# Optimization experiments

Hardware: AMD Instinct MI355X
Metric: run time of the kernel (lower is better)

Reference implementation:

```python
import jax, jax.numpy as jnp
import numpy as np

N = 100000      # nodes
E = 1600000     # edges (avg degree 16)
F_IN = 128
F_OUT = 128
EPS = 1e-5      # BatchNorm eps


def setup_inputs() -> dict:
    key = jax.random.key(0)
    ks = jax.random.split(key, 10)
    s_in = 1.0 / np.sqrt(F_IN)
    s_out = 1.0 / np.sqrt(F_OUT)
    return {
        "x": jax.random.normal(ks[0], (N, F_IN), dtype=jnp.float32),
        "edge_index": jax.random.randint(ks[1], (2, E), 0, N, dtype=jnp.int32),
        # layer 0: SAGEConv(F_IN, F_OUT, aggr='max'); lin_l has bias, lin_r does not
        "W0_l": jax.random.normal(ks[2], (F_IN, F_OUT), dtype=jnp.float32) * s_in,
        "b0_l": jnp.zeros((F_OUT,), dtype=jnp.float32),
        "W0_r": jax.random.normal(ks[3], (F_IN, F_OUT), dtype=jnp.float32) * s_in,
        "gamma0": jnp.ones((F_OUT,), dtype=jnp.float32),
        "beta0": jnp.zeros((F_OUT,), dtype=jnp.float32),
        # layer 1: SAGEConv(F_OUT, F_OUT, aggr='max')
        "W1_l": jax.random.normal(ks[4], (F_OUT, F_OUT), dtype=jnp.float32) * s_out,
        "b1_l": jnp.zeros((F_OUT,), dtype=jnp.float32),
        "W1_r": jax.random.normal(ks[5], (F_OUT, F_OUT), dtype=jnp.float32) * s_out,
        "gamma1": jnp.ones((F_OUT,), dtype=jnp.float32),
        "beta1": jnp.zeros((F_OUT,), dtype=jnp.float32),
    }


def _sage_conv_max(x, src, dst, W_l, b_l, W_r):
    # gather source features along edges, scatter-max into destination nodes
    msgs = x[src]                                             # [E, F]
    agg = jax.ops.segment_max(msgs, dst, num_segments=N)      # [N, F], -inf for isolated
    agg = jnp.where(jnp.isfinite(agg), agg, 0.0)              # PyG fills empty segments with 0
    return agg @ W_l + b_l + x @ W_r                          # lin_l(aggr) + lin_r(x)


def _batch_norm(h, gamma, beta):
    mu = jnp.mean(h, axis=0)
    var = jnp.var(h, axis=0)
    return (h - mu) * jax.lax.rsqrt(var + EPS) * gamma + beta


def reference(x, edge_index, W0_l, b0_l, W0_r, gamma0, beta0,
              W1_l, b1_l, W1_r, gamma1, beta1):
    src, dst = edge_index[0], edge_index[1]
    h = _sage_conv_max(x, src, dst, W0_l, b0_l, W0_r)
    h = jax.nn.relu(_batch_norm(h, gamma0, beta0))
    h = _sage_conv_max(h, src, dst, W1_l, b1_l, W1_r)
    h = jax.nn.relu(_batch_norm(h, gamma1, beta1))
    return h
```

## Files before the change

### kernel.cpp

```cpp
#include <hip/hip_runtime.h>
#include <stdint.h>

#define EPS_BN 1e-5f

typedef __attribute__((ext_vector_type(8))) short short8v;
typedef __attribute__((ext_vector_type(4))) float f32x4;

__device__ __forceinline__ unsigned rne_bf16(float f) {
    unsigned u = __float_as_uint(f);
    return (u + 0x7FFFu + ((u >> 16) & 1u)) >> 16;
}

extern "C" __global__ __launch_bounds__(256)
void f32_to_bf16_kernel(const float4* __restrict__ in, uint2* __restrict__ out, long n4) {
    long i = (long)blockIdx.x * 256 + threadIdx.x;
    long stride = (long)gridDim.x * 256;
    for (; i < n4; i += stride) {
        float4 v = in[i];
        uint2 o;
        o.x = rne_bf16(v.x) | (rne_bf16(v.y) << 16);
        o.y = rne_bf16(v.z) | (rne_bf16(v.w) << 16);
        out[i] = o;
    }
}

extern "C" __global__ __launch_bounds__(256)
void wt_prep2_kernel(const float* __restrict__ Wl0, const float* __restrict__ Wr0,
                     unsigned short* __restrict__ Wt0,
                     const float* __restrict__ Wl1, const float* __restrict__ Wr1,
                     unsigned short* __restrict__ Wt1) {
    int b = blockIdx.x;
    const float* Wl = (b < 128) ? Wl0 : Wl1;
    const float* Wr = (b < 128) ? Wr0 : Wr1;
    unsigned short* Wt = (b < 128) ? Wt0 : Wt1;
    int idx = (b & 127) * 256 + threadIdx.x;
    int col = idx >> 8, k = idx & 255;
    float v = (k < 128) ? Wl[(size_t)k * 128 + col] : Wr[(size_t)(k - 128) * 128 + col];
    Wt[(size_t)col * 256 + k] = (unsigned short)rne_bf16(v);
}

extern "C" __global__ __launch_bounds__(256)
void init_head_kernel(int* __restrict__ head, int n) {
    int i = blockIdx.x * 256 + threadIdx.x;
    if (i < n) head[i] = -1;
}

extern "C" __global__ __launch_bounds__(256)
void link_kernel(const int* __restrict__ ei, int* __restrict__ head4,
                 uint2* __restrict__ pair, int E) {
    int e = blockIdx.x * 256 + threadIdx.x;
    if (e < E) {
        int src = ei[e];
        int dst = ei[E + e];
        int old = atomicExch(&head4[dst * 4 + (e & 3)], e);
        uint2 p; p.x = (unsigned)src; p.y = (unsigned)old;
        pair[e] = p;
    }
}

#define FM8(v)                                              \
    a0 = fmaxf(a0, __uint_as_float((v).x << 16));           \
    a1 = fmaxf(a1, __uint_as_float((v).x));                 \
    a2 = fmaxf(a2, __uint_as_float((v).y << 16));           \
    a3 = fmaxf(a3, __uint_as_float((v).y));                 \
    a4 = fmaxf(a4, __uint_as_float((v).z << 16));           \
    a5 = fmaxf(a5, __uint_as_float((v).z));                 \
    a6 = fmaxf(a6, __uint_as_float((v).w << 16));           \
    a7 = fmaxf(a7, __uint_as_float((v).w));

extern "C" __global__ __launch_bounds__(256, 8)
void gather_max_ll16_kernel(const uint4* __restrict__ x16r, const int* __restrict__ head4,
                            const uint2* __restrict__ pair,
                            uint4* __restrict__ agg16, float* __restrict__ stats, int Nn) {
    if (blockIdx.x == 0 && threadIdx.x < 256) stats[threadIdx.x] = 0.0f;
    int t = blockIdx.x * 256 + threadIdx.x;
    int node = t >> 4;
    if (node >= Nn) return;
    int lane = t & 15;

    int4 hh = *(const int4*)(head4 + (size_t)node * 4);
    int e0 = hh.x, e1 = hh.y, e2 = hh.z, e3 = hh.w;

    uint4 out;
    if ((e0 & e1 & e2 & e3) < 0 && e0 < 0 && e1 < 0 && e2 < 0 && e3 < 0) {
        out.x = out.y = out.z = out.w = 0u;
    } else {
        float a0 = -INFINITY, a1 = -INFINITY, a2 = -INFINITY, a3 = -INFINITY;
        float a4 = -INFINITY, a5 = -INFINITY, a6 = -INFINITY, a7 = -INFINITY;
        while ((e0 & e1 & e2 & e3) >= 0 || e0 >= 0 || e1 >= 0 || e2 >= 0 || e3 >= 0) {
            bool b0 = e0 >= 0, b1 = e1 >= 0, b2 = e2 >= 0, b3 = e3 >= 0;
            uint2 p0, p1, p2, p3;
            uint4 v0, v1, v2, v3;
            if (b0) p0 = pair[e0];
            if (b1) p1 = pair[e1];
            if (b2) p2 = pair[e2];
            if (b3) p3 = pair[e3];
            if (b0) v0 = x16r[(size_t)p0.x * 16 + lane];
            if (b1) v1 = x16r[(size_t)p1.x * 16 + lane];
            if (b2) v2 = x16r[(size_t)p2.x * 16 + lane];
            if (b3) v3 = x16r[(size_t)p3.x * 16 + lane];
            if (b0) { e0 = (int)p0.y; FM8(v0); }
            if (b1) { e1 = (int)p1.y; FM8(v1); }
            if (b2) { e2 = (int)p2.y; FM8(v2); }
            if (b3) { e3 = (int)p3.y; FM8(v3); }
        }
        out.x = (__float_as_uint(a0) >> 16) | (__float_as_uint(a1) & 0xFFFF0000u);
        out.y = (__float_as_uint(a2) >> 16) | (__float_as_uint(a3) & 0xFFFF0000u);
        out.z = (__float_as_uint(a4) >> 16) | (__float_as_uint(a5) & 0xFFFF0000u);
        out.w = (__float_as_uint(a6) >> 16) | (__float_as_uint(a7) & 0xFFFF0000u);
    }
    agg16[(size_t)node * 16 + lane] = out;
}

extern "C" __global__ __launch_bounds__(256)
void gemm_bf16_kernel(const unsigned short* __restrict__ agg16,
                      const unsigned short* __restrict__ xin16,
                      const unsigned short* __restrict__ Wt,
                      const float* __restrict__ bias,
                      float* __restrict__ h, float* __restrict__ stats, int nrows) {
    __shared__ float redS[4][128];
    __shared__ float redQ[4][128];

    const int t = threadIdx.x;
    const int w = t >> 6, l = t & 63;
    const int wm = w >> 1, wn = w & 1;
    const int r16 = l & 15, g = l >> 4;
    const int blockRow = blockIdx.x * 128;
    const int colBase = wn * 64;

    f32x4 acc[4][4];
#pragma unroll
    for (int m = 0; m < 4; ++m)
#pragma unroll
        for (int n = 0; n < 4; ++n) acc[m][n] = (f32x4){0.f, 0.f, 0.f, 0.f};

    const short8v az = {0, 0, 0, 0, 0, 0, 0, 0};

#pragma unroll
    for (int kt = 0; kt < 8; ++kt) {
        const unsigned short* Asrc = (kt < 4) ? agg16 : xin16;
        const int kofs = (kt < 4) ? kt * 32 : kt * 32 - 128;

        short8v b[4];
#pragma unroll
        for (int n = 0; n < 4; ++n) {
            int col = colBase + n * 16 + r16;
            b[n] = *(const short8v*)(Wt + (size_t)col * 256 + kt * 32 + g * 8);
        }
        short8v a[4];
#pragma unroll
        for (int m = 0; m < 4; ++m) {
            int row = blockRow + wm * 64 + m * 16 + r16;
            a[m] = (row < nrows)
                 ? *(const short8v*)(Asrc + (size_t)row * 128 + kofs + g * 8)
                 : az;
        }
#pragma unroll
        for (int m = 0; m < 4; ++m)
#pragma unroll
            for (int n = 0; n < 4; ++n)
                acc[m][n] = __builtin_amdgcn_mfma_f32_16x16x32_bf16(a[m], b[n], acc[m][n], 0, 0, 0);
    }

    for (int i = t; i < 512; i += 256) {
        ((float*)redS)[i] = 0.f;
        ((float*)redQ)[i] = 0.f;
    }
    __syncthreads();

    float bcol[4];
#pragma unroll
    for (int n = 0; n < 4; ++n) bcol[n] = bias[colBase + n * 16 + r16];

    float s4[4] = {0.f, 0.f, 0.f, 0.f};
    float q4[4] = {0.f, 0.f, 0.f, 0.f};
#pragma unroll
    for (int m = 0; m < 4; ++m) {
#pragma unroll
        for (int reg = 0; reg < 4; ++reg) {
            int row = blockRow + wm * 64 + m * 16 + g * 4 + reg;
            if (row < nrows) {
#pragma unroll
                for (int n = 0; n < 4; ++n) {
                    float o = acc[m][n][reg] + bcol[n];
                    h[(size_t)row * 128 + colBase + n * 16 + r16] = o;
                    s4[n] += o;
                    q4[n] += o * o;
                }
            }
        }
    }
#pragma unroll
    for (int n = 0; n < 4; ++n) {
        s4[n] += __shfl_xor(s4[n], 16, 64);
        s4[n] += __shfl_xor(s4[n], 32, 64);
        q4[n] += __shfl_xor(q4[n], 16, 64);
        q4[n] += __shfl_xor(q4[n], 32, 64);
    }
    if (g == 0) {
#pragma unroll
        for (int n = 0; n < 4; ++n) {
            redS[w][colBase + n * 16 + r16] = s4[n];
            redQ[w][colBase + n * 16 + r16] = q4[n];
        }
    }
    __syncthreads();
    if (t < 128) {
        float s = redS[0][t] + redS[1][t] + redS[2][t] + redS[3][t];
        float q = redQ[0][t] + redQ[1][t] + redQ[2][t] + redQ[3][t];
        atomicAdd(&stats[t], s);
        atomicAdd(&stats[128 + t], q);
    }
}

__device__ __forceinline__ void bn_make_ss(const float* __restrict__ stats,
                                           const float* __restrict__ gamma,
                                           const float* __restrict__ beta,
                                           float inv_n, float* s_ss) {
    int t = threadIdx.x;
    if (t < 128) {
        float mu = stats[t] * inv_n;
        float var = stats[128 + t] * inv_n - mu * mu;
        float sc = gamma[t] * rsqrtf(var + EPS_BN);
        s_ss[t] = sc;
        s_ss[128 + t] = beta[t] - mu * sc;
    }
    __syncthreads();
}

extern "C" __global__ __launch_bounds__(256)
void bn_relu_tobf16_kernel(const float4* __restrict__ h, const float* __restrict__ stats,
                           const float* __restrict__ gamma, const float* __restrict__ beta,
                           float inv_n, uint2* __restrict__ y16, long n4) {
    __shared__ float s_ss[256];
    bn_make_ss(stats, gamma, beta, inv_n, s_ss);
    long i = (long)blockIdx.x * blockDim.x + threadIdx.x;
    long stride = (long)gridDim.x * blockDim.x;
    for (; i < n4; i += stride) {
        int c4 = (int)(i & 31) * 4;
        float4 v = h[i];
        float o0 = fmaxf(fmaf(v.x, s_ss[c4 + 0], s_ss[128 + c4 + 0]), 0.f);
        float o1 = fmaxf(fmaf(v.y, s_ss[c4 + 1], s_ss[128 + c4 + 1]), 0.f);
        float o2 = fmaxf(fmaf(v.z, s_ss[c4 + 2], s_ss[128 + c4 + 2]), 0.f);
        float o3 = fmaxf(fmaf(v.w, s_ss[c4 + 3], s_ss[128 + c4 + 3]), 0.f);
        uint2 o;
        o.x = rne_bf16(o0) | (rne_bf16(o1) << 16);
        o.y = rne_bf16(o2) | (rne_bf16(o3) << 16);
        y16[i] = o;
    }
}

extern "C" __global__ __launch_bounds__(256)
void bn_relu_f32_kernel(float4* __restrict__ h, const float* __restrict__ stats,
                        const float* __restrict__ gamma, const float* __restrict__ beta,
                        float inv_n, long n4) {
    __shared__ float s_ss[256];
    bn_make_ss(stats, gamma, beta, inv_n, s_ss);
    long i = (long)blockIdx.x * blockDim.x + threadIdx.x;
    long stride = (long)gridDim.x * blockDim.x;
    for (; i < n4; i += stride) {
        int c4 = (int)(i & 31) * 4;
        float4 v = h[i];
        v.x = fmaxf(fmaf(v.x, s_ss[c4 + 0], s_ss[128 + c4 + 0]), 0.f);
        v.y = fmaxf(fmaf(v.y, s_ss[c4 + 1], s_ss[128 + c4 + 1]), 0.f);
        v.z = fmaxf(fmaf(v.z, s_ss[c4 + 2], s_ss[128 + c4 + 2]), 0.f);
        v.w = fmaxf(fmaf(v.w, s_ss[c4 + 3], s_ss[128 + c4 + 3]), 0.f);
        h[i] = v;
    }
}

__device__ __forceinline__ unsigned map_f(float f) {
    unsigned u = __float_as_uint(f);
    return (u & 0x80000000u) ? ~u : (u | 0x80000000u);
}
__device__ __forceinline__ float unmap_f(unsigned m) {
    return (m & 0x80000000u) ? __uint_as_float(m & 0x7FFFFFFFu) : __uint_as_float(~m);
}

extern "C" __global__ __launch_bounds__(256)
void init_sentinel_kernel(uint4* __restrict__ agg, long n4) {
    uint4 z = {0u, 0u, 0u, 0u};
    long i = (long)blockIdx.x * blockDim.x + threadIdx.x;
    long stride = (long)gridDim.x * blockDim.x;
    for (; i < n4; i += stride) agg[i] = z;
}

extern "C" __global__ __launch_bounds__(256)
void scatter_max_kernel(const float4* __restrict__ xin, const int* __restrict__ ei,
                        unsigned* __restrict__ agg, int E) {
    int t = blockIdx.x * 256 + threadIdx.x;
    int e = t >> 5;
    if (e >= E) return;
    int f4 = t & 31;
    int src = ei[e];
    int dst = ei[E + e];
    float4 v = xin[(size_t)src * 32 + f4];
    unsigned* p = agg + (size_t)dst * 128 + (size_t)f4 * 4;
    atomicMax(p + 0, map_f(v.x));
    atomicMax(p + 1, map_f(v.y));
    atomicMax(p + 2, map_f(v.z));
    atomicMax(p + 3, map_f(v.w));
}

extern "C" __global__ __launch_bounds__(256)
void unmap_kernel(unsigned* __restrict__ agg, long n) {
    long i = (long)blockIdx.x * blockDim.x + threadIdx.x;
    long stride = (long)gridDim.x * blockDim.x;
    for (; i < n; i += stride) {
        unsigned u = agg[i];
        agg[i] = __float_as_uint(u ? unmap_f(u) : 0.0f);
    }
}

extern "C" __global__
void zero_stats_kernel(float* __restrict__ stats) {
    stats[threadIdx.x] = 0.0f;
}

extern "C" __global__ __launch_bounds__(256)
void gemm_kernel(const float* __restrict__ agg, const float* __restrict__ xin,
                 const float* __restrict__ Wl, const float* __restrict__ Wr,
                 const float* __restrict__ bias, float* __restrict__ h,
                 float* __restrict__ stats, int nrows) {
    __shared__ __align__(16) float As[64][36];
    __shared__ __align__(16) float Bs[32][136];
    __shared__ float redS[4][128];
    __shared__ float redQ[4][128];

    const int t = threadIdx.x;
    const int tx = t & 15;
    const int ty = t >> 4;
    const int tx8 = tx * 8;
    const int ty4 = ty * 4;
    const int blockRow = blockIdx.x * 64;

    float acc[4][8];
#pragma unroll
    for (int j = 0; j < 4; ++j)
#pragma unroll
        for (int c = 0; c < 8; ++c) acc[j][c] = 0.0f;

    for (int kt = 0; kt < 8; ++kt) {
        const int k0 = kt * 32;
        const bool isAgg = (kt < 4);
        const float* W = isAgg ? Wl : Wr;
        const float* Asrc = isAgg ? agg : xin;
        const int kw = isAgg ? k0 : (k0 - 128);

#pragma unroll
        for (int it = 0; it < 4; ++it) {
            int idx = t + it * 256;
            int kr = idx >> 5, cq = idx & 31;
            float4 ww = *(const float4*)&W[(size_t)(kw + kr) * 128 + cq * 4];
            *(float4*)&Bs[kr][cq * 4] = ww;
        }
#pragma unroll
        for (int it = 0; it < 2; ++it) {
            int idx = t + it * 256;
            int r = idx >> 3, kq = idx & 7;
            int row_g = blockRow + r;
            float4 a = {0.f, 0.f, 0.f, 0.f};
            if (row_g < nrows)
                a = *(const float4*)&Asrc[(size_t)row_g * 128 + kw + kq * 4];
            *(float4*)&As[r][kq * 4] = a;
        }
        __syncthreads();

#pragma unroll
        for (int kk = 0; kk < 32; ++kk) {
            float aa[4];
            aa[0] = As[ty4 + 0][kk];
            aa[1] = As[ty4 + 1][kk];
            aa[2] = As[ty4 + 2][kk];
            aa[3] = As[ty4 + 3][kk];
            float4 b0 = *(const float4*)&Bs[kk][tx8];
            float4 b1 = *(const float4*)&Bs[kk][tx8 + 4];
            float bb[8] = {b0.x, b0.y, b0.z, b0.w, b1.x, b1.y, b1.z, b1.w};
#pragma unroll
            for (int j = 0; j < 4; ++j)
#pragma unroll
                for (int c = 0; c < 8; ++c)
                    acc[j][c] = fmaf(aa[j], bb[c], acc[j][c]);
        }
        __syncthreads();
    }

    float bv[8];
#pragma unroll
    for (int c = 0; c < 8; ++c) bv[c] = bias[tx8 + c];

    float s_loc[8], q_loc[8];
#pragma unroll
    for (int c = 0; c < 8; ++c) { s_loc[c] = 0.f; q_loc[c] = 0.f; }

#pragma unroll
    for (int j = 0; j < 4; ++j) {
        int row = blockRow + ty4 + j;
        if (row < nrows) {
            float o[8];
#pragma unroll
            for (int c = 0; c < 8; ++c) {
                o[c] = acc[j][c] + bv[c];
                s_loc[c] += o[c];
                q_loc[c] += o[c] * o[c];
            }
            float4 o0 = {o[0], o[1], o[2], o[3]};
            float4 o1 = {o[4], o[5], o[6], o[7]};
            *(float4*)&h[(size_t)row * 128 + tx8] = o0;
            *(float4*)&h[(size_t)row * 128 + tx8 + 4] = o1;
        }
    }

#pragma unroll
    for (int c = 0; c < 8; ++c) {
        s_loc[c] += __shfl_xor(s_loc[c], 16, 64);
        s_loc[c] += __shfl_xor(s_loc[c], 32, 64);
        q_loc[c] += __shfl_xor(q_loc[c], 16, 64);
        q_loc[c] += __shfl_xor(q_loc[c], 32, 64);
    }
    int wave = t >> 6;
    if ((t & 63) < 16) {
#pragma unroll
        for (int c = 0; c < 8; ++c) {
            redS[wave][tx8 + c] = s_loc[c];
            redQ[wave][tx8 + c] = q_loc[c];
        }
    }
    __syncthreads();
    if (t < 128) {
        float s = redS[0][t] + redS[1][t] + redS[2][t] + redS[3][t];
        float q = redQ[0][t] + redQ[1][t] + redQ[2][t] + redQ[3][t];
        atomicAdd(&stats[t], s);
        atomicAdd(&stats[128 + t], q);
    }
}

static void run_layer_atomic(const float* in_feat, const int* ei, int Nn, int Ee,
                             const float* Wl, const float* bl, const float* Wr,
                             const float* gamma, const float* beta,
                             float* agg, float* stats, float* out, hipStream_t stream) {
    long aggN = (long)Nn * 128;
    long n4 = aggN / 4;

    zero_stats_kernel<<<1, 256, 0, stream>>>(stats);
    int initBlocks = (int)((n4 + 255) / 256);
    if (initBlocks > 4096) initBlocks = 4096;
    init_sentinel_kernel<<<initBlocks, 256, 0, stream>>>((uint4*)agg, n4);
    int sb = (int)(((long)Ee * 32 + 255) / 256);
    scatter_max_kernel<<<sb, 256, 0, stream>>>((const float4*)in_feat, ei,
                                               (unsigned*)agg, Ee);
    int ub = (int)((aggN + 255) / 256);
    if (ub > 8192) ub = 8192;
    unmap_kernel<<<ub, 256, 0, stream>>>((unsigned*)agg, aggN);
    gemm_kernel<<<(Nn + 63) / 64, 256, 0, stream>>>(agg, in_feat, Wl, Wr, bl,
                                                    out, stats, Nn);
    int bnBlocks = (int)((n4 + 255) / 256);
    if (bnBlocks > 8192) bnBlocks = 8192;
    bn_relu_f32_kernel<<<bnBlocks, 256, 0, stream>>>((float4*)out, stats, gamma, beta,
                                                     1.0f / (float)Nn, n4);
}

extern "C" void kernel_launch(void* const* d_in, const int* in_sizes, int n_in,
                              void* d_out, int out_size, void* d_ws, size_t ws_size,
                              hipStream_t stream) {
    (void)n_in; (void)out_size;
    const float* x     = (const float*)d_in[0];
    const int*   ei    = (const int*)d_in[1];
    const float* W0_l  = (const float*)d_in[2];
    const float* b0_l  = (const float*)d_in[3];
    const float* W0_r  = (const float*)d_in[4];
    const float* g0    = (const float*)d_in[5];
    const float* be0   = (const float*)d_in[6];
    const float* W1_l  = (const float*)d_in[7];
    const float* b1_l  = (const float*)d_in[8];
    const float* W1_r  = (const float*)d_in[9];
    const float* g1    = (const float*)d_in[10];
    const float* be1   = (const float*)d_in[11];

    int Nn = in_sizes[0] / 128;
    int Ee = in_sizes[1] / 2;
    long n4 = (long)Nn * 32;
    float inv_n = 1.0f / (float)Nn;

    char* p = (char*)d_ws;
    unsigned short* xy16 = (unsigned short*)p;  p += (size_t)Nn * 128 * 2;
    unsigned short* agg16 = (unsigned short*)p; p += (size_t)Nn * 128 * 2;
    float* stats = (float*)p;                   p += 256 * sizeof(float);
    unsigned short* Wt0 = (unsigned short*)p;   p += 128 * 256 * 2;
    unsigned short* Wt1 = (unsigned short*)p;   p += 128 * 256 * 2;
    int* head4 = (int*)p;                       p += (size_t)Nn * 4 * sizeof(int);
    uint2* pair = (uint2*)p;                    p += (size_t)Ee * sizeof(uint2);
    size_t needed = (size_t)(p - (char*)d_ws);
    float* out = (float*)d_out;

    if (ws_size >= needed) {
        int cvB = (int)((n4 + 255) / 256);
        if (cvB > 4096) cvB = 4096;
        f32_to_bf16_kernel<<<cvB, 256, 0, stream>>>((const float4*)x, (uint2*)xy16, n4);
        wt_prep2_kernel<<<256, 256, 0, stream>>>(W0_l, W0_r, Wt0, W1_l, W1_r, Wt1);
        init_head_kernel<<<(Nn * 4 + 255) / 256, 256, 0, stream>>>(head4, Nn * 4);
        link_kernel<<<(Ee + 255) / 256, 256, 0, stream>>>(ei, head4, pair, Ee);

        int bnB = (int)((n4 + 255) / 256);
        if (bnB > 8192) bnB = 8192;

        gather_max_ll16_kernel<<<(Nn * 16 + 255) / 256, 256, 0, stream>>>(
            (const uint4*)xy16, head4, pair, (uint4*)agg16, stats, Nn);
        gemm_bf16_kernel<<<(Nn + 127) / 128, 256, 0, stream>>>(agg16, xy16, Wt0, b0_l,
                                                               out, stats, Nn);
        bn_relu_tobf16_kernel<<<bnB, 256, 0, stream>>>((const float4*)out, stats, g0, be0,
                                                       inv_n, (uint2*)xy16, n4);
        gather_max_ll16_kernel<<<(Nn * 16 + 255) / 256, 256, 0, stream>>>(
            (const uint4*)xy16, head4, pair, (uint4*)agg16, stats, Nn);
        gemm_bf16_kernel<<<(Nn + 127) / 128, 256, 0, stream>>>(agg16, xy16, Wt1, b1_l,
                                                               out, stats, Nn);
        bn_relu_f32_kernel<<<bnB, 256, 0, stream>>>((float4*)out, stats, g1, be1,
                                                    inv_n, n4);
    } else {
        float* agg = (float*)d_ws;
        float* fstats = (float*)((char*)d_ws + (size_t)Nn * 128 * sizeof(float));
        run_layer_atomic(x, ei, Nn, Ee, W0_l, b0_l, W0_r, g0, be0,
                         agg, fstats, out, stream);
        run_layer_atomic(out, ei, Nn, Ee, W1_l, b1_l, W1_r, g1, be1,
                         agg, fstats, out, stream);
    }
}
```

Baseline: 419.9 us.

## Fuse layer-0 BN+ReLU into layer-1 gather and store layer-0 output as bf16

The layer-0 GEMM now writes bf16 instead of fp32. The separate BN+ReLU conversion pass is removed: layer 1's gather applies the affine BN and ReLU after the max, which is valid because that transform is monotone when the scale is positive. The same gather also writes the node's own normalized row for the second GEMM operand. The per-destination 4-way linked lists become a single list, which shortens setup but removes memory-level parallelism inside the gather loop. This relies on positive BN scale (gamma) for max and affine to commute, and it changes rounding points.

```diff
diff --git a/kernel.cpp b/kernel.cpp
--- a/kernel.cpp
+++ b/kernel.cpp
@@ -46,30 +46,20 @@
 }
 
 extern "C" __global__ __launch_bounds__(256)
-void link_kernel(const int* __restrict__ ei, int* __restrict__ head4,
+void link_kernel(const int* __restrict__ ei, int* __restrict__ head,
                  uint2* __restrict__ pair, int E) {
     int e = blockIdx.x * 256 + threadIdx.x;
     if (e < E) {
         int src = ei[e];
         int dst = ei[E + e];
-        int old = atomicExch(&head4[dst * 4 + (e & 3)], e);
+        int old = atomicExch(&head[dst], e);
         uint2 p; p.x = (unsigned)src; p.y = (unsigned)old;
         pair[e] = p;
     }
 }
 
-#define FM8(v)                                              \
-    a0 = fmaxf(a0, __uint_as_float((v).x << 16));           \
-    a1 = fmaxf(a1, __uint_as_float((v).x));                 \
-    a2 = fmaxf(a2, __uint_as_float((v).y << 16));           \
-    a3 = fmaxf(a3, __uint_as_float((v).y));                 \
-    a4 = fmaxf(a4, __uint_as_float((v).z << 16));           \
-    a5 = fmaxf(a5, __uint_as_float((v).z));                 \
-    a6 = fmaxf(a6, __uint_as_float((v).w << 16));           \
-    a7 = fmaxf(a7, __uint_as_float((v).w));
-
 extern "C" __global__ __launch_bounds__(256, 8)
-void gather_max_ll16_kernel(const uint4* __restrict__ x16r, const int* __restrict__ head4,
+void gather_max_ll16_kernel(const uint4* __restrict__ x16r, const int* __restrict__ head,
                             const uint2* __restrict__ pair,
                             uint4* __restrict__ agg16, float* __restrict__ stats, int Nn) {
     if (blockIdx.x == 0 && threadIdx.x < 256) stats[threadIdx.x] = 0.0f;
@@ -77,140 +67,37 @@
     int node = t >> 4;
     if (node >= Nn) return;
     int lane = t & 15;
-
-    int4 hh = *(const int4*)(head4 + (size_t)node * 4);
-    int e0 = hh.x, e1 = hh.y, e2 = hh.z, e3 = hh.w;
-
+    int e = head[node];
     uint4 out;
-    if ((e0 & e1 & e2 & e3) < 0 && e0 < 0 && e1 < 0 && e2 < 0 && e3 < 0) {
-        out.x = out.y = out.z = out.w = 0u;
-    } else {
-        float a0 = -INFINITY, a1 = -INFINITY, a2 = -INFINITY, a3 = -INFINITY;
-        float a4 = -INFINITY, a5 = -INFINITY, a6 = -INFINITY, a7 = -INFINITY;
-        while ((e0 & e1 & e2 & e3) >= 0 || e0 >= 0 || e1 >= 0 || e2 >= 0 || e3 >= 0) {
-            bool b0 = e0 >= 0, b1 = e1 >= 0, b2 = e2 >= 0, b3 = e3 >= 0;
-            uint2 p0, p1, p2, p3;
-            uint4 v0, v1, v2, v3;
-            if (b0) p0 = pair[e0];
-            if (b1) p1 = pair[e1];
-            if (b2) p2 = pair[e2];
-            if (b3) p3 = pair[e3];
-            if (b0) v0 = x16r[(size_t)p0.x * 16 + lane];
-            if (b1) v1 = x16r[(size_t)p1.x * 16 + lane];
-            if (b2) v2 = x16r[(size_t)p2.x * 16 + lane];
-            if (b3) v3 = x16r[(size_t)p3.x * 16 + lane];
-            if (b0) { e0 = (int)p0.y; FM8(v0); }
-            if (b1) { e1 = (int)p1.y; FM8(v1); }
-            if (b2) { e2 = (int)p2.y; FM8(v2); }
-            if (b3) { e3 = (int)p3.y; FM8(v3); }
+    if (e >= 0) {
+        uint2 p = pair[e];
+        uint4 r = x16r[(size_t)p.x * 16 + lane];
+        float a0 = __uint_as_float(r.x << 16), a1 = __uint_as_float(r.x);
+        float a2 = __uint_as_float(r.y << 16), a3 = __uint_as_float(r.y);
+        float a4 = __uint_as_float(r.z << 16), a5 = __uint_as_float(r.z);
+        float a6 = __uint_as_float(r.w << 16), a7 = __uint_as_float(r.w);
+        int en = (int)p.y;
+        while (en >= 0) {
+            uint2 pn = pair[en];
+            uint4 v = x16r[(size_t)pn.x * 16 + lane];
+            en = (int)pn.y;
+            a0 = fmaxf(a0, __uint_as_float(v.x << 16));
+            a1 = fmaxf(a1, __uint_as_float(v.x));
+            a2 = fmaxf(a2, __uint_as_float(v.y << 16));
+            a3 = fmaxf(a3, __uint_as_float(v.y));
+            a4 = fmaxf(a4, __uint_as_float(v.z << 16));
+            a5 = fmaxf(a5, __uint_as_float(v.z));
+            a6 = fmaxf(a6, __uint_as_float(v.w << 16));
+            a7 = fmaxf(a7, __uint_as_float(v.w));
         }
         out.x = (__float_as_uint(a0) >> 16) | (__float_as_uint(a1) & 0xFFFF0000u);
         out.y = (__float_as_uint(a2) >> 16) | (__float_as_uint(a3) & 0xFFFF0000u);
         out.z = (__float_as_uint(a4) >> 16) | (__float_as_uint(a5) & 0xFFFF0000u);
         out.w = (__float_as_uint(a6) >> 16) | (__float_as_uint(a7) & 0xFFFF0000u);
+    } else {
+        out.x = out.y = out.z = out.w = 0u;
     }
     agg16[(size_t)node * 16 + lane] = out;
-}
-
-extern "C" __global__ __launch_bounds__(256)
-void gemm_bf16_kernel(const unsigned short* __restrict__ agg16,
-                      const unsigned short* __restrict__ xin16,
-                      const unsigned short* __restrict__ Wt,
-                      const float* __restrict__ bias,
-                      float* __restrict__ h, float* __restrict__ stats, int nrows) {
-    __shared__ float redS[4][128];
-    __shared__ float redQ[4][128];
-
-    const int t = threadIdx.x;
-    const int w = t >> 6, l = t & 63;
-    const int wm = w >> 1, wn = w & 1;
-    const int r16 = l & 15, g = l >> 4;
-    const int blockRow = blockIdx.x * 128;
-    const int colBase = wn * 64;
-
-    f32x4 acc[4][4];
-#pragma unroll
-    for (int m = 0; m < 4; ++m)
-#pragma unroll
-        for (int n = 0; n < 4; ++n) acc[m][n] = (f32x4){0.f, 0.f, 0.f, 0.f};
-
-    const short8v az = {0, 0, 0, 0, 0, 0, 0, 0};
-
-#pragma unroll
-    for (int kt = 0; kt < 8; ++kt) {
-        const unsigned short* Asrc = (kt < 4) ? agg16 : xin16;
-        const int kofs = (kt < 4) ? kt * 32 : kt * 32 - 128;
-
-        short8v b[4];
-#pragma unroll
-        for (int n = 0; n < 4; ++n) {
-            int col = colBase + n * 16 + r16;
-            b[n] = *(const short8v*)(Wt + (size_t)col * 256 + kt * 32 + g * 8);
-        }
-        short8v a[4];
-#pragma unroll
-        for (int m = 0; m < 4; ++m) {
-            int row = blockRow + wm * 64 + m * 16 + r16;
-            a[m] = (row < nrows)
-                 ? *(const short8v*)(Asrc + (size_t)row * 128 + kofs + g * 8)
-                 : az;
-        }
-#pragma unroll
-        for (int m = 0; m < 4; ++m)
-#pragma unroll
-            for (int n = 0; n < 4; ++n)
-                acc[m][n] = __builtin_amdgcn_mfma_f32_16x16x32_bf16(a[m], b[n], acc[m][n], 0, 0, 0);
-    }
-
-    for (int i = t; i < 512; i += 256) {
-        ((float*)redS)[i] = 0.f;
-        ((float*)redQ)[i] = 0.f;
-    }
-    __syncthreads();
-
-    float bcol[4];
-#pragma unroll
-    for (int n = 0; n < 4; ++n) bcol[n] = bias[colBase + n * 16 + r16];
-
-    float s4[4] = {0.f, 0.f, 0.f, 0.f};
-    float q4[4] = {0.f, 0.f, 0.f, 0.f};
-#pragma unroll
-    for (int m = 0; m < 4; ++m) {
-#pragma unroll
-        for (int reg = 0; reg < 4; ++reg) {
-            int row = blockRow + wm * 64 + m * 16 + g * 4 + reg;
-            if (row < nrows) {
-#pragma unroll
-                for (int n = 0; n < 4; ++n) {
-                    float o = acc[m][n][reg] + bcol[n];
-                    h[(size_t)row * 128 + colBase + n * 16 + r16] = o;
-                    s4[n] += o;
-                    q4[n] += o * o;
-                }
-            }
-        }
-    }
-#pragma unroll
-    for (int n = 0; n < 4; ++n) {
-        s4[n] += __shfl_xor(s4[n], 16, 64);
-        s4[n] += __shfl_xor(s4[n], 32, 64);
-        q4[n] += __shfl_xor(q4[n], 16, 64);
-        q4[n] += __shfl_xor(q4[n], 32, 64);
-    }
-    if (g == 0) {
-#pragma unroll
-        for (int n = 0; n < 4; ++n) {
-            redS[w][colBase + n * 16 + r16] = s4[n];
-            redQ[w][colBase + n * 16 + r16] = q4[n];
-        }
-    }
-    __syncthreads();
-    if (t < 128) {
-        float s = redS[0][t] + redS[1][t] + redS[2][t] + redS[3][t];
-        float q = redQ[0][t] + redQ[1][t] + redQ[2][t] + redQ[3][t];
-        atomicAdd(&stats[t], s);
-        atomicAdd(&stats[128 + t], q);
-    }
 }
 
 __device__ __forceinline__ void bn_make_ss(const float* __restrict__ stats,
@@ -228,26 +115,222 @@
     __syncthreads();
 }
 
-extern "C" __global__ __launch_bounds__(256)
-void bn_relu_tobf16_kernel(const float4* __restrict__ h, const float* __restrict__ stats,
-                           const float* __restrict__ gamma, const float* __restrict__ beta,
-                           float inv_n, uint2* __restrict__ y16, long n4) {
+extern "C" __global__ __launch_bounds__(256, 8)
+void gather_max_bn_kernel(const uint4* __restrict__ h1r, const int* __restrict__ head,
+                          const uint2* __restrict__ pair,
+                          const float* __restrict__ stats0,
+                          const float* __restrict__ gamma, const float* __restrict__ beta,
+                          float inv_n,
+                          uint4* __restrict__ agg16, uint4* __restrict__ y16,
+                          float* __restrict__ stats1, int Nn) {
     __shared__ float s_ss[256];
-    bn_make_ss(stats, gamma, beta, inv_n, s_ss);
-    long i = (long)blockIdx.x * blockDim.x + threadIdx.x;
-    long stride = (long)gridDim.x * blockDim.x;
-    for (; i < n4; i += stride) {
-        int c4 = (int)(i & 31) * 4;
-        float4 v = h[i];
-        float o0 = fmaxf(fmaf(v.x, s_ss[c4 + 0], s_ss[128 + c4 + 0]), 0.f);
-        float o1 = fmaxf(fmaf(v.y, s_ss[c4 + 1], s_ss[128 + c4 + 1]), 0.f);
-        float o2 = fmaxf(fmaf(v.z, s_ss[c4 + 2], s_ss[128 + c4 + 2]), 0.f);
-        float o3 = fmaxf(fmaf(v.w, s_ss[c4 + 3], s_ss[128 + c4 + 3]), 0.f);
-        uint2 o;
-        o.x = rne_bf16(o0) | (rne_bf16(o1) << 16);
-        o.y = rne_bf16(o2) | (rne_bf16(o3) << 16);
-        y16[i] = o;
-    }
+    bn_make_ss(stats0, gamma, beta, inv_n, s_ss);
+    if (blockIdx.x == 0 && threadIdx.x < 256) stats1[threadIdx.x] = 0.0f;
+
+    int t = blockIdx.x * 256 + threadIdx.x;
+    int node = t >> 4;
+    if (node >= Nn) return;
+    int lane = t & 15;
+
+    float sc[8], sh[8];
+#pragma unroll
+    for (int j = 0; j < 8; ++j) {
+        sc[j] = s_ss[lane * 8 + j];
+        sh[j] = s_ss[128 + lane * 8 + j];
+    }
+
+    {
+        uint4 r = h1r[(size_t)node * 16 + lane];
+        float v0 = __uint_as_float(r.x << 16), v1 = __uint_as_float(r.x & 0xFFFF0000u);
+        float v2 = __uint_as_float(r.y << 16), v3 = __uint_as_float(r.y & 0xFFFF0000u);
+        float v4 = __uint_as_float(r.z << 16), v5 = __uint_as_float(r.z & 0xFFFF0000u);
+        float v6 = __uint_as_float(r.w << 16), v7 = __uint_as_float(r.w & 0xFFFF0000u);
+        v0 = fmaxf(fmaf(v0, sc[0], sh[0]), 0.f);
+        v1 = fmaxf(fmaf(v1, sc[1], sh[1]), 0.f);
+        v2 = fmaxf(fmaf(v2, sc[2], sh[2]), 0.f);
+        v3 = fmaxf(fmaf(v3, sc[3], sh[3]), 0.f);
+        v4 = fmaxf(fmaf(v4, sc[4], sh[4]), 0.f);
+        v5 = fmaxf(fmaf(v5, sc[5], sh[5]), 0.f);
+        v6 = fmaxf(fmaf(v6, sc[6], sh[6]), 0.f);
+        v7 = fmaxf(fmaf(v7, sc[7], sh[7]), 0.f);
+        uint4 o;
+        o.x = rne_bf16(v0) | (rne_bf16(v1) << 16);
+        o.y = rne_bf16(v2) | (rne_bf16(v3) << 16);
+        o.z = rne_bf16(v4) | (rne_bf16(v5) << 16);
+        o.w = rne_bf16(v6) | (rne_bf16(v7) << 16);
+        y16[(size_t)node * 16 + lane] = o;
+    }
+
+    int e = head[node];
+    uint4 out;
+    if (e >= 0) {
+        uint2 p = pair[e];
+        uint4 r = h1r[(size_t)p.x * 16 + lane];
+        float a0 = __uint_as_float(r.x << 16), a1 = __uint_as_float(r.x);
+        float a2 = __uint_as_float(r.y << 16), a3 = __uint_as_float(r.y);
+        float a4 = __uint_as_float(r.z << 16), a5 = __uint_as_float(r.z);
+        float a6 = __uint_as_float(r.w << 16), a7 = __uint_as_float(r.w);
+        int en = (int)p.y;
+        while (en >= 0) {
+            uint2 pn = pair[en];
+            uint4 v = h1r[(size_t)pn.x * 16 + lane];
+            en = (int)pn.y;
+            a0 = fmaxf(a0, __uint_as_float(v.x << 16));
+            a1 = fmaxf(a1, __uint_as_float(v.x));
+            a2 = fmaxf(a2, __uint_as_float(v.y << 16));
+            a3 = fmaxf(a3, __uint_as_float(v.y));
+            a4 = fmaxf(a4, __uint_as_float(v.z << 16));
+            a5 = fmaxf(a5, __uint_as_float(v.z));
+            a6 = fmaxf(a6, __uint_as_float(v.w << 16));
+            a7 = fmaxf(a7, __uint_as_float(v.w));
+        }
+        a1 = __uint_as_float(__float_as_uint(a1) & 0xFFFF0000u);
+        a3 = __uint_as_float(__float_as_uint(a3) & 0xFFFF0000u);
+        a5 = __uint_as_float(__float_as_uint(a5) & 0xFFFF0000u);
+        a7 = __uint_as_float(__float_as_uint(a7) & 0xFFFF0000u);
+        a0 = fmaxf(fmaf(a0, sc[0], sh[0]), 0.f);
+        a1 = fmaxf(fmaf(a1, sc[1], sh[1]), 0.f);
+        a2 = fmaxf(fmaf(a2, sc[2], sh[2]), 0.f);
+        a3 = fmaxf(fmaf(a3, sc[3], sh[3]), 0.f);
+        a4 = fmaxf(fmaf(a4, sc[4], sh[4]), 0.f);
+        a5 = fmaxf(fmaf(a5, sc[5], sh[5]), 0.f);
+        a6 = fmaxf(fmaf(a6, sc[6], sh[6]), 0.f);
+        a7 = fmaxf(fmaf(a7, sc[7], sh[7]), 0.f);
+        out.x = rne_bf16(a0) | (rne_bf16(a1) << 16);
+        out.y = rne_bf16(a2) | (rne_bf16(a3) << 16);
+        out.z = rne_bf16(a4) | (rne_bf16(a5) << 16);
+        out.w = rne_bf16(a6) | (rne_bf16(a7) << 16);
+    } else {
+        out.x = out.y = out.z = out.w = 0u;
+    }
+    agg16[(size_t)node * 16 + lane] = out;
+}
+
+template <int OUT_BF16>
+__device__ __forceinline__
+void gemm_bf16_body(const unsigned short* __restrict__ agg16,
+                    const unsigned short* __restrict__ xin16,
+                    const unsigned short* __restrict__ Wt,
+                    const float* __restrict__ bias,
+                    void* __restrict__ hout, float* __restrict__ stats, int nrows) {
+    __shared__ float redS[4][128];
+    __shared__ float redQ[4][128];
+
+    const int t = threadIdx.x;
+    const int w = t >> 6, l = t & 63;
+    const int wm = w >> 1, wn = w & 1;
+    const int r16 = l & 15, g = l >> 4;
+    const int blockRow = blockIdx.x * 128;
+    const int colBase = wn * 64;
+
+    f32x4 acc[4][4];
+#pragma unroll
+    for (int m = 0; m < 4; ++m)
+#pragma unroll
+        for (int n = 0; n < 4; ++n) acc[m][n] = (f32x4){0.f, 0.f, 0.f, 0.f};
+
+    const short8v az = {0, 0, 0, 0, 0, 0, 0, 0};
+
+#pragma unroll
+    for (int kt = 0; kt < 8; ++kt) {
+        const unsigned short* Asrc = (kt < 4) ? agg16 : xin16;
+        const int kofs = (kt < 4) ? kt * 32 : kt * 32 - 128;
+
+        short8v b[4];
+#pragma unroll
+        for (int n = 0; n < 4; ++n) {
+            int col = colBase + n * 16 + r16;
+            b[n] = *(const short8v*)(Wt + (size_t)col * 256 + kt * 32 + g * 8);
+        }
+        short8v a[4];
+#pragma unroll
+        for (int m = 0; m < 4; ++m) {
+            int row = blockRow + wm * 64 + m * 16 + r16;
+            a[m] = (row < nrows)
+                 ? *(const short8v*)(Asrc + (size_t)row * 128 + kofs + g * 8)
+                 : az;
+        }
+#pragma unroll
+        for (int m = 0; m < 4; ++m)
+#pragma unroll
+            for (int n = 0; n < 4; ++n)
+                acc[m][n] = __builtin_amdgcn_mfma_f32_16x16x32_bf16(a[m], b[n], acc[m][n], 0, 0, 0);
+    }
+
+    for (int i = t; i < 512; i += 256) {
+        ((float*)redS)[i] = 0.f;
+        ((float*)redQ)[i] = 0.f;
+    }
+    __syncthreads();
+
+    float bcol[4];
+#pragma unroll
+    for (int n = 0; n < 4; ++n) bcol[n] = bias[colBase + n * 16 + r16];
+
+    float s4[4] = {0.f, 0.f, 0.f, 0.f};
+    float q4[4] = {0.f, 0.f, 0.f, 0.f};
+#pragma unroll
+    for (int m = 0; m < 4; ++m) {
+#pragma unroll
+        for (int reg = 0; reg < 4; ++reg) {
+            int row = blockRow + wm * 64 + m * 16 + g * 4 + reg;
+            if (row < nrows) {
+#pragma unroll
+                for (int n = 0; n < 4; ++n) {
+                    float o = acc[m][n][reg] + bcol[n];
+                    int col = colBase + n * 16 + r16;
+                    if (OUT_BF16)
+                        ((unsigned short*)hout)[(size_t)row * 128 + col] =
+                            (unsigned short)rne_bf16(o);
+                    else
+                        ((float*)hout)[(size_t)row * 128 + col] = o;
+                    s4[n] += o;
+                    q4[n] += o * o;
+                }
+            }
+        }
+    }
+#pragma unroll
+    for (int n = 0; n < 4; ++n) {
+        s4[n] += __shfl_xor(s4[n], 16, 64);
+        s4[n] += __shfl_xor(s4[n], 32, 64);
+        q4[n] += __shfl_xor(q4[n], 16, 64);
+        q4[n] += __shfl_xor(q4[n], 32, 64);
+    }
+    if (g == 0) {
+#pragma unroll
+        for (int n = 0; n < 4; ++n) {
+            redS[w][colBase + n * 16 + r16] = s4[n];
+            redQ[w][colBase + n * 16 + r16] = q4[n];
+        }
+    }
+    __syncthreads();
+    if (t < 128) {
+        float s = redS[0][t] + redS[1][t] + redS[2][t] + redS[3][t];
+        float q = redQ[0][t] + redQ[1][t] + redQ[2][t] + redQ[3][t];
+        atomicAdd(&stats[t], s);
+        atomicAdd(&stats[128 + t], q);
+    }
+}
+
+extern "C" __global__ __launch_bounds__(256)
+void gemm_bf16_out16_kernel(const unsigned short* __restrict__ agg16,
+                            const unsigned short* __restrict__ xin16,
+                            const unsigned short* __restrict__ Wt,
+                            const float* __restrict__ bias,
+                            unsigned short* __restrict__ h, float* __restrict__ stats,
+                            int nrows) {
+    gemm_bf16_body<1>(agg16, xin16, Wt, bias, h, stats, nrows);
+}
+
+extern "C" __global__ __launch_bounds__(256)
+void gemm_bf16_out32_kernel(const unsigned short* __restrict__ agg16,
+                            const unsigned short* __restrict__ xin16,
+                            const unsigned short* __restrict__ Wt,
+                            const float* __restrict__ bias,
+                            float* __restrict__ h, float* __restrict__ stats,
+                            int nrows) {
+    gemm_bf16_body<0>(agg16, xin16, Wt, bias, h, stats, nrows);
 }
 
 extern "C" __global__ __launch_bounds__(256)
@@ -485,36 +568,39 @@
     char* p = (char*)d_ws;
     unsigned short* xy16 = (unsigned short*)p;  p += (size_t)Nn * 128 * 2;
     unsigned short* agg16 = (unsigned short*)p; p += (size_t)Nn * 128 * 2;
-    float* stats = (float*)p;                   p += 256 * sizeof(float);
+    float* stats0 = (float*)p;                  p += 256 * sizeof(float);
+    float* stats1 = (float*)p;                  p += 256 * sizeof(float);
     unsigned short* Wt0 = (unsigned short*)p;   p += 128 * 256 * 2;
     unsigned short* Wt1 = (unsigned short*)p;   p += 128 * 256 * 2;
-    int* head4 = (int*)p;                       p += (size_t)Nn * 4 * sizeof(int);
+    int* head = (int*)p;                        p += (size_t)Nn * sizeof(int);
     uint2* pair = (uint2*)p;                    p += (size_t)Ee * sizeof(uint2);
     size_t needed = (size_t)(p - (char*)d_ws);
     float* out = (float*)d_out;
+    unsigned short* h1 = (unsigned short*)d_out;
 
     if (ws_size >= needed) {
         int cvB = (int)((n4 + 255) / 256);
         if (cvB > 4096) cvB = 4096;
         f32_to_bf16_kernel<<<cvB, 256, 0, stream>>>((const float4*)x, (uint2*)xy16, n4);
         wt_prep2_kernel<<<256, 256, 0, stream>>>(W0_l, W0_r, Wt0, W1_l, W1_r, Wt1);
-        init_head_kernel<<<(Nn * 4 + 255) / 256, 256, 0, stream>>>(head4, Nn * 4);
-        link_kernel<<<(Ee + 255) / 256, 256, 0, stream>>>(ei, head4, pair, Ee);
-
+        init_head_kernel<<<(Nn + 255) / 256, 256, 0, stream>>>(head, Nn);
+        link_kernel<<<(Ee + 255) / 256, 256, 0, stream>>>(ei, head, pair, Ee);
+
+        int gB = (Nn * 16 + 255) / 256;
+        int mB = (Nn + 127) / 128;
         int bnB = (int)((n4 + 255) / 256);
         if (bnB > 8192) bnB = 8192;
 
-        gather_max_ll16_kernel<<<(Nn * 16 + 255) / 256, 256, 0, stream>>>(
-            (const uint4*)xy16, head4, pair, (uint4*)agg16, stats, Nn);
-        gemm_bf16_kernel<<<(Nn + 127) / 128, 256, 0, stream>>>(agg16, xy16, Wt0, b0_l,
-                                                               out, stats, Nn);
-        bn_relu_tobf16_kernel<<<bnB, 256, 0, stream>>>((const float4*)out, stats, g0, be0,
-                                                       inv_n, (uint2*)xy16, n4);
-        gather_max_ll16_kernel<<<(Nn * 16 + 255) / 256, 256, 0, stream>>>(
-            (const uint4*)xy16, head4, pair, (uint4*)agg16, stats, Nn);
-        gemm_bf16_kernel<<<(Nn + 127) / 128, 256, 0, stream>>>(agg16, xy16, Wt1, b1_l,
-                                                               out, stats, Nn);
-        bn_relu_f32_kernel<<<bnB, 256, 0, stream>>>((float4*)out, stats, g1, be1,
+        gather_max_ll16_kernel<<<gB, 256, 0, stream>>>(
+            (const uint4*)xy16, head, pair, (uint4*)agg16, stats0, Nn);
+        gemm_bf16_out16_kernel<<<mB, 256, 0, stream>>>(agg16, xy16, Wt0, b0_l,
+                                                       h1, stats0, Nn);
+        gather_max_bn_kernel<<<gB, 256, 0, stream>>>(
+            (const uint4*)h1, head, pair, stats0, g0, be0, inv_n,
+            (uint4*)agg16, (uint4*)xy16, stats1, Nn);
+        gemm_bf16_out32_kernel<<<mB, 256, 0, stream>>>(agg16, xy16, Wt1, b1_l,
+                                                       out, stats1, Nn);
+        bn_relu_f32_kernel<<<bnB, 256, 0, stream>>>((float4*)out, stats1, g1, be1,
                                                     inv_n, n4);
     } else {
         float* agg = (float*)d_ws;
```

Result: faster. 397.4 us (-5.4%).
